# Kernel optimization log

Hardware: AMD Instinct MI355X
Metric: run time of the kernel (lower is better)

The kernel has to match this reference:

```python
import jax, jax.numpy as jnp
import numpy as np

TAU = 20.0   # membrane time constant (init default)
TH = 1.0     # spike threshold (init default)
K = 10.0     # surrogate sigmoid slope (hard-coded in forward)
EPS = 1e-6


def setup_inputs() -> dict:
    key = jax.random.key(0)
    I = jax.random.normal(key, (4096, 4096), dtype=jnp.float32)  # [B, L]
    return {"I": I}


def reference(I):
    B, L = I.shape

    def step(v, I_t):
        # Euler: dv = -v/tau + I ; v <- v + dv
        v = v - v / TAU + I_t
        s_soft = jax.nn.sigmoid(K * (v - TH))
        s_hard = (v >= TH).astype(I.dtype)
        # straight-through: value = s_hard, gradient flows through s_soft
        s = jax.lax.stop_gradient(s_hard - s_soft) + s_soft
        # reset: v <- v * (1 - stopgrad(s)); stopgrad(s) has value s_hard
        v = v * (1.0 - s_hard)
        return v, (s, s_hard)

    v0 = jnp.zeros((B,), dtype=I.dtype)
    _, (spikes_t, hard_t) = jax.lax.scan(step, v0, I.T)  # xs: [L, B]
    spikes = spikes_t.T       # [B, L]
    hard_spikes = hard_t.T    # [B, L]

    # hard latency: index of first hard spike, else L
    fired = hard_spikes > 0.5
    has = jnp.any(fired, axis=1)
    idx = jnp.argmax(fired, axis=1)
    hard_latency = jnp.where(has, idx, L).astype(jnp.int32)  # [B]

    # soft latency: spike-weighted mean time
    time = jnp.arange(L, dtype=spikes.dtype)
    w = spikes / (spikes.sum(axis=1, keepdims=True) + EPS)
    soft_latency = (w * time).sum(axis=1)  # [B]

    return spikes, hard_latency, soft_latency
```

## Files before the change

### kernel.cpp

```cpp
#include <hip/hip_runtime.h>

#define B_DIM 4096
#define L_DIM 4096
#define SEGLEN 256
#define NSEG (L_DIM / SEGLEN)
#define WARM 512
#define CHUNK 64
#define CF4 (CHUNK / 4)
#define LSTRIDE 68

__global__ __launch_bounds__(256) void init_kernel(float* wsf, int* wsi) {
    int i = blockIdx.x * 256 + threadIdx.x;
    if (i < 2 * B_DIM) wsf[i] = 0.f;
    if (i < B_DIM) wsi[i] = L_DIM;
}

#define LIF_CORE(IIN)                         \
    float q0 = u * cdiv;                      \
    float rr = fmaf(-20.0f, q0, u);           \
    float q  = fmaf(rr, cdiv, q0);            \
    float a  = u - q;                         \
    float b  = a + (IIN);                     \
    u = sp ? (IIN) : b;                       \
    sp = (u >= 1.0f);

#define WARM_STEP(IIN) { LIF_CORE(IIN) }

#define FULL_STEP(IIN, SOUT)                  \
    {                                         \
        LIF_CORE(IIN)                         \
        float sf = sp ? 1.0f : 0.0f;          \
        cnt += sf;                            \
        seen = fmaxf(seen, sf);               \
        accS += cnt;                          \
        accF += seen;                         \
        (SOUT) = sf;                          \
    }

__global__ __launch_bounds__(128, 1) void lif_kernel(const float* __restrict__ I,
                                                     float* __restrict__ out,
                                                     float* __restrict__ Cacc,
                                                     float* __restrict__ tsAcc,
                                                     int* __restrict__ firstAcc) {
    __shared__ __align__(16) float lds[2][64 * LSTRIDE];
    const int wid = threadIdx.x >> 6;
    const int lane = threadIdx.x & 63;
    const int seg = blockIdx.x >> 6;
    const int rowBase = (blockIdx.x & 63) * 64;
    const int t0 = seg * SEGLEN;
    const int start = (t0 > WARM) ? (t0 - WARM) : 0;
    const int nwarmCh = (t0 - start) / CHUNK;
    const int nch = nwarmCh + SEGLEN / CHUNK;

    if (wid == 1) {
        const int srow = lane >> 4, scol = lane & 15;
        const float* gb = I + (size_t)rowBase * L_DIM + start + scol * 4;
        {
            float* dst = &lds[0][0];
#pragma unroll
            for (int p = 0; p < 16; ++p) {
                const int r = 4 * p + srow;
                float4 v = *(const float4*)(gb + (size_t)r * L_DIM);
                *(float4*)&dst[r * LSTRIDE + scol * 4] = v;
            }
        }
        __syncthreads();
        for (int c = 0; c < nch; ++c) {
            if (c + 1 < nch) {
                const float* g = gb + (c + 1) * CHUNK;
                float* dst = &lds[(c + 1) & 1][0];
#pragma unroll
                for (int p = 0; p < 16; ++p) {
                    const int r = 4 * p + srow;
                    float4 v = *(const float4*)(g + (size_t)r * L_DIM);
                    *(float4*)&dst[r * LSTRIDE + scol * 4] = v;
                }
            }
            __syncthreads();
        }
    } else {
        const int row = rowBase + lane;
        float u = 0.f, cnt = 0.f, seen = 0.f, accS = 0.f, accF = 0.f;
        bool sp = false;
        const float cdiv = 0.05f;
        float* so = out + (size_t)row * L_DIM + t0;

        __syncthreads();
        for (int c = 0; c < nch; ++c) {
            const float* buf = &lds[c & 1][lane * LSTRIDE];
            float4 R[CF4];
#pragma unroll
            for (int j = 0; j < CF4; ++j) R[j] = *(const float4*)(buf + 4 * j);

            if (c < nwarmCh) {
#pragma unroll
                for (int j = 0; j < CF4; ++j) {
                    float4 iv = R[j];
                    WARM_STEP(iv.x) WARM_STEP(iv.y) WARM_STEP(iv.z) WARM_STEP(iv.w)
                }
            } else {
                float* sd = so + (c - nwarmCh) * CHUNK;
#pragma unroll
                for (int j = 0; j < CF4; ++j) {
                    float4 iv = R[j];
                    float4 sv;
                    FULL_STEP(iv.x, sv.x) FULL_STEP(iv.y, sv.y)
                    FULL_STEP(iv.z, sv.z) FULL_STEP(iv.w, sv.w)
                    *(float4*)(sd + 4 * j) = sv;
                }
            }
            __syncthreads();
        }

        if (cnt > 0.f) {
            const int firstLocal = (int)((float)SEGLEN - accF);
            atomicMin(&firstAcc[row], t0 + firstLocal);
        }
        atomicAdd(&Cacc[row], cnt);
        atomicAdd(&tsAcc[row], fmaf((float)(t0 + SEGLEN), cnt, -accS));
    }
}

__global__ __launch_bounds__(256) void fin_kernel(const float* __restrict__ Cacc,
                                                  const float* __restrict__ tsAcc,
                                                  const int* __restrict__ firstAcc,
                                                  float* __restrict__ out) {
    int r = blockIdx.x * 256 + threadIdx.x;
    if (r < B_DIM) {
        out[(size_t)B_DIM * L_DIM + r] = (float)firstAcc[r];
        out[(size_t)B_DIM * L_DIM + B_DIM + r] = tsAcc[r] / (Cacc[r] + 1e-6f);
    }
}

extern "C" void kernel_launch(void* const* d_in, const int* in_sizes, int n_in,
                              void* d_out, int out_size, void* d_ws, size_t ws_size,
                              hipStream_t stream) {
    const float* I = (const float*)d_in[0];
    float* out = (float*)d_out;
    float* wsf = (float*)d_ws;
    int* wsi = (int*)((float*)d_ws + 2 * B_DIM);
    (void)in_sizes; (void)n_in; (void)out_size; (void)ws_size;

    init_kernel<<<(2 * B_DIM + 255) / 256, 256, 0, stream>>>(wsf, wsi);
    lif_kernel<<<NSEG * 64, 128, 0, stream>>>(I, out, wsf, wsf + B_DIM, wsi);
    fin_kernel<<<(B_DIM + 255) / 256, 256, 0, stream>>>(wsf, wsf + B_DIM, wsi, out);
}
```

Before: 140.1 us.

## Stage spike outputs through LDS and store coalesced from the loader wave

Compute lanes now write spike values back into their LDS input buffer instead of storing straight to global memory with a per-row stride. On the next iteration the loader wave reads the finished chunk from LDS and writes it out as row-coalesced float4 stores, with a final flush after the loop. This is meant to replace strided, uncoalesced per-thread global stores with coalesced ones and take the store work off the compute wave. In exchange the loader wave does extra LDS traffic and more work between barriers, which may lengthen each synchronized step.

```diff
diff --git a/kernel.cpp b/kernel.cpp
--- a/kernel.cpp
+++ b/kernel.cpp
@@ -55,6 +55,7 @@
     if (wid == 1) {
         const int srow = lane >> 4, scol = lane & 15;
         const float* gb = I + (size_t)rowBase * L_DIM + start + scol * 4;
+        float* ob = out + (size_t)rowBase * L_DIM + t0 + scol * 4;
         {
             float* dst = &lds[0][0];
 #pragma unroll
@@ -66,6 +67,22 @@
         }
         __syncthreads();
         for (int c = 0; c < nch; ++c) {
+            const int cp = c - 1;
+            if (cp >= nwarmCh) {
+                float* sb = &lds[cp & 1][0];
+                float4 S[16];
+#pragma unroll
+                for (int p = 0; p < 16; ++p) {
+                    const int r = 4 * p + srow;
+                    S[p] = *(const float4*)&sb[r * LSTRIDE + scol * 4];
+                }
+                float* og = ob + (size_t)(cp - nwarmCh) * CHUNK;
+#pragma unroll
+                for (int p = 0; p < 16; ++p) {
+                    const int r = 4 * p + srow;
+                    *(float4*)(og + (size_t)r * L_DIM) = S[p];
+                }
+            }
             if (c + 1 < nch) {
                 const float* g = gb + (c + 1) * CHUNK;
                 float* dst = &lds[(c + 1) & 1][0];
@@ -78,16 +95,26 @@
             }
             __syncthreads();
         }
+        {
+            const int cp = nch - 1;
+            float* sb = &lds[cp & 1][0];
+            float* og = ob + (size_t)(cp - nwarmCh) * CHUNK;
+#pragma unroll
+            for (int p = 0; p < 16; ++p) {
+                const int r = 4 * p + srow;
+                float4 v = *(const float4*)&sb[r * LSTRIDE + scol * 4];
+                *(float4*)(og + (size_t)r * L_DIM) = v;
+            }
+        }
     } else {
         const int row = rowBase + lane;
         float u = 0.f, cnt = 0.f, seen = 0.f, accS = 0.f, accF = 0.f;
         bool sp = false;
         const float cdiv = 0.05f;
-        float* so = out + (size_t)row * L_DIM + t0;
 
         __syncthreads();
         for (int c = 0; c < nch; ++c) {
-            const float* buf = &lds[c & 1][lane * LSTRIDE];
+            float* buf = &lds[c & 1][lane * LSTRIDE];
             float4 R[CF4];
 #pragma unroll
             for (int j = 0; j < CF4; ++j) R[j] = *(const float4*)(buf + 4 * j);
@@ -99,14 +126,13 @@
                     WARM_STEP(iv.x) WARM_STEP(iv.y) WARM_STEP(iv.z) WARM_STEP(iv.w)
                 }
             } else {
-                float* sd = so + (c - nwarmCh) * CHUNK;
 #pragma unroll
                 for (int j = 0; j < CF4; ++j) {
                     float4 iv = R[j];
                     float4 sv;
                     FULL_STEP(iv.x, sv.x) FULL_STEP(iv.y, sv.y)
                     FULL_STEP(iv.z, sv.z) FULL_STEP(iv.w, sv.w)
-                    *(float4*)(sd + 4 * j) = sv;
+                    *(float4*)(buf + 4 * j) = sv;
                 }
             }
             __syncthreads();
```

New measurement: 129.9 us. 1.08x faster.

## Make each wave load, compute and store its own segment with register prefetch

Applied to the files above, without the earlier changes.

The producer/consumer wave split is replaced: each of the two waves in a block now handles its own time segment of the same 64 rows. Each wave prefetches the next chunk into registers, transposes through a private LDS buffer without block barriers, and writes spikes back through LDS as coalesced row-wise float4 stores. The goal is to double the number of compute waves, remove __syncthreads stalls and fix the strided per-lane output stores. In exchange it uses more registers per wave, and the extra LDS round-trips sit on the serial path.

```diff
diff --git a/kernel.cpp b/kernel.cpp
--- a/kernel.cpp
+++ b/kernel.cpp
@@ -45,80 +45,86 @@
     __shared__ __align__(16) float lds[2][64 * LSTRIDE];
     const int wid = threadIdx.x >> 6;
     const int lane = threadIdx.x & 63;
-    const int seg = blockIdx.x >> 6;
-    const int rowBase = (blockIdx.x & 63) * 64;
+    float* buf = &lds[wid][0];
+
+    const int rowBase = (blockIdx.x >> 3) * 64;
+    const int seg = ((blockIdx.x & 7) << 1) + wid;
     const int t0 = seg * SEGLEN;
     const int start = (t0 > WARM) ? (t0 - WARM) : 0;
     const int nwarmCh = (t0 - start) / CHUNK;
     const int nch = nwarmCh + SEGLEN / CHUNK;
 
-    if (wid == 1) {
-        const int srow = lane >> 4, scol = lane & 15;
-        const float* gb = I + (size_t)rowBase * L_DIM + start + scol * 4;
-        {
-            float* dst = &lds[0][0];
+    const int srow = lane >> 4, scol = lane & 15;
+    const float* gb = I + (size_t)rowBase * L_DIM + start + scol * 4;
+    float* ob = out + (size_t)rowBase * L_DIM + t0 + scol * 4;
+
+    const int row = rowBase + lane;
+    float u = 0.f, cnt = 0.f, seen = 0.f, accS = 0.f, accF = 0.f;
+    bool sp = false;
+    const float cdiv = 0.05f;
+
+    float4 G[16], R[16];
+
 #pragma unroll
-            for (int p = 0; p < 16; ++p) {
-                const int r = 4 * p + srow;
-                float4 v = *(const float4*)(gb + (size_t)r * L_DIM);
-                *(float4*)&dst[r * LSTRIDE + scol * 4] = v;
+    for (int p = 0; p < 16; ++p)
+        G[p] = *(const float4*)(gb + (size_t)(4 * p + srow) * L_DIM);
+#pragma unroll
+    for (int p = 0; p < 16; ++p)
+        *(float4*)&buf[(4 * p + srow) * LSTRIDE + scol * 4] = G[p];
+#pragma unroll
+    for (int j = 0; j < 16; ++j)
+        R[j] = *(const float4*)&buf[lane * LSTRIDE + 4 * j];
+
+    for (int c = 0; c < nch; ++c) {
+        if (c + 1 < nch) {
+            const float* g = gb + (c + 1) * CHUNK;
+#pragma unroll
+            for (int p = 0; p < 16; ++p)
+                G[p] = *(const float4*)(g + (size_t)(4 * p + srow) * L_DIM);
+        }
+        __builtin_amdgcn_sched_barrier(0);
+
+        if (c < nwarmCh) {
+#pragma unroll
+            for (int j = 0; j < 16; ++j) {
+                float4 iv = R[j];
+                WARM_STEP(iv.x) WARM_STEP(iv.y) WARM_STEP(iv.z) WARM_STEP(iv.w)
             }
-        }
-        __syncthreads();
-        for (int c = 0; c < nch; ++c) {
-            if (c + 1 < nch) {
-                const float* g = gb + (c + 1) * CHUNK;
-                float* dst = &lds[(c + 1) & 1][0];
+        } else {
 #pragma unroll
-                for (int p = 0; p < 16; ++p) {
-                    const int r = 4 * p + srow;
-                    float4 v = *(const float4*)(g + (size_t)r * L_DIM);
-                    *(float4*)&dst[r * LSTRIDE + scol * 4] = v;
-                }
+            for (int j = 0; j < 16; ++j) {
+                float4 iv = R[j];
+                float4 sv;
+                FULL_STEP(iv.x, sv.x) FULL_STEP(iv.y, sv.y)
+                FULL_STEP(iv.z, sv.z) FULL_STEP(iv.w, sv.w)
+                *(float4*)&buf[lane * LSTRIDE + 4 * j] = sv;
             }
-            __syncthreads();
-        }
-    } else {
-        const int row = rowBase + lane;
-        float u = 0.f, cnt = 0.f, seen = 0.f, accS = 0.f, accF = 0.f;
-        bool sp = false;
-        const float cdiv = 0.05f;
-        float* so = out + (size_t)row * L_DIM + t0;
-
-        __syncthreads();
-        for (int c = 0; c < nch; ++c) {
-            const float* buf = &lds[c & 1][lane * LSTRIDE];
-            float4 R[CF4];
+            float4 S[16];
+            float* og = ob + (size_t)(c - nwarmCh) * CHUNK;
 #pragma unroll
-            for (int j = 0; j < CF4; ++j) R[j] = *(const float4*)(buf + 4 * j);
-
-            if (c < nwarmCh) {
+            for (int p = 0; p < 16; ++p)
+                S[p] = *(const float4*)&buf[(4 * p + srow) * LSTRIDE + scol * 4];
 #pragma unroll
-                for (int j = 0; j < CF4; ++j) {
-                    float4 iv = R[j];
-                    WARM_STEP(iv.x) WARM_STEP(iv.y) WARM_STEP(iv.z) WARM_STEP(iv.w)
-                }
-            } else {
-                float* sd = so + (c - nwarmCh) * CHUNK;
-#pragma unroll
-                for (int j = 0; j < CF4; ++j) {
-                    float4 iv = R[j];
-                    float4 sv;
-                    FULL_STEP(iv.x, sv.x) FULL_STEP(iv.y, sv.y)
-                    FULL_STEP(iv.z, sv.z) FULL_STEP(iv.w, sv.w)
-                    *(float4*)(sd + 4 * j) = sv;
-                }
-            }
-            __syncthreads();
+            for (int p = 0; p < 16; ++p)
+                *(float4*)(og + (size_t)(4 * p + srow) * L_DIM) = S[p];
         }
 
-        if (cnt > 0.f) {
-            const int firstLocal = (int)((float)SEGLEN - accF);
-            atomicMin(&firstAcc[row], t0 + firstLocal);
+        if (c + 1 < nch) {
+#pragma unroll
+            for (int p = 0; p < 16; ++p)
+                *(float4*)&buf[(4 * p + srow) * LSTRIDE + scol * 4] = G[p];
+#pragma unroll
+            for (int j = 0; j < 16; ++j)
+                R[j] = *(const float4*)&buf[lane * LSTRIDE + 4 * j];
         }
-        atomicAdd(&Cacc[row], cnt);
-        atomicAdd(&tsAcc[row], fmaf((float)(t0 + SEGLEN), cnt, -accS));
     }
+
+    if (cnt > 0.f) {
+        const int firstLocal = (int)((float)SEGLEN - accF);
+        atomicMin(&firstAcc[row], t0 + firstLocal);
+    }
+    atomicAdd(&Cacc[row], cnt);
+    atomicAdd(&tsAcc[row], fmaf((float)(t0 + SEGLEN), cnt, -accS));
 }
 
 __global__ __launch_bounds__(256) void fin_kernel(const float* __restrict__ Cacc,
@@ -142,6 +148,6 @@
     (void)in_sizes; (void)n_in; (void)out_size; (void)ws_size;
 
     init_kernel<<<(2 * B_DIM + 255) / 256, 256, 0, stream>>>(wsf, wsi);
-    lif_kernel<<<NSEG * 64, 128, 0, stream>>>(I, out, wsf, wsf + B_DIM, wsi);
+    lif_kernel<<<(NSEG / 2) * 64, 128, 0, stream>>>(I, out, wsf, wsf + B_DIM, wsi);
     fin_kernel<<<(B_DIM + 255) / 256, 256, 0, stream>>>(wsf, wsf + B_DIM, wsi, out);
 }
```

Result: slower. 191.1 us (+36.4%).

## Use direct global-to-LDS loads so every wave computes its own segment

Applied to the files above, without the earlier changes.

The dedicated producer wave is removed. Each of the two waves in a block now handles its own time segment, prefetching the next chunk straight into LDS with global_load_lds in an XOR-swizzled layout and waiting on vmcnt instead of __syncthreads. Spike outputs are staged back through the LDS buffer so rows are written with coalesced float4 stores. Half as many blocks are launched, and the compute lanes per block double. The price is hand-tuned waitcnt logic that is fragile, plus wave-private LDS reuse that relies on in-order completion.

```diff
diff --git a/kernel.cpp b/kernel.cpp
--- a/kernel.cpp
+++ b/kernel.cpp
@@ -6,8 +6,7 @@
 #define NSEG (L_DIM / SEGLEN)
 #define WARM 512
 #define CHUNK 64
-#define CF4 (CHUNK / 4)
-#define LSTRIDE 68
+#define LROW 64
 
 __global__ __launch_bounds__(256) void init_kernel(float* wsf, int* wsi) {
     int i = blockIdx.x * 256 + threadIdx.x;
@@ -37,88 +36,116 @@
         (SOUT) = sf;                          \
     }
 
+typedef const __attribute__((address_space(1))) void g_void;
+typedef __attribute__((address_space(3))) void l_void;
+__device__ __forceinline__ void gll16(const float* src, float* ldsbase) {
+    __builtin_amdgcn_global_load_lds((g_void*)src, (l_void*)ldsbase, 16, 0, 0);
+}
+
 __global__ __launch_bounds__(128, 1) void lif_kernel(const float* __restrict__ I,
                                                      float* __restrict__ out,
                                                      float* __restrict__ Cacc,
                                                      float* __restrict__ tsAcc,
                                                      int* __restrict__ firstAcc) {
-    __shared__ __align__(16) float lds[2][64 * LSTRIDE];
+    __shared__ __align__(16) float lds[2][2][64 * LROW];
     const int wid = threadIdx.x >> 6;
     const int lane = threadIdx.x & 63;
-    const int seg = blockIdx.x >> 6;
-    const int rowBase = (blockIdx.x & 63) * 64;
+    float* buf0 = &lds[wid][0][0];
+    float* buf1 = &lds[wid][1][0];
+
+    const int rowBase = (blockIdx.x >> 3) * 64;
+    const int seg = ((blockIdx.x & 7) << 1) + wid;
     const int t0 = seg * SEGLEN;
     const int start = (t0 > WARM) ? (t0 - WARM) : 0;
     const int nwarmCh = (t0 - start) / CHUNK;
     const int nch = nwarmCh + SEGLEN / CHUNK;
 
-    if (wid == 1) {
-        const int srow = lane >> 4, scol = lane & 15;
-        const float* gb = I + (size_t)rowBase * L_DIM + start + scol * 4;
-        {
-            float* dst = &lds[0][0];
+    const int srow = lane >> 4, scol = lane & 15;
+    const float* gbase = I + (size_t)rowBase * L_DIM + start;
+
+    const int row = rowBase + lane;
+    float u = 0.f, cnt = 0.f, seen = 0.f, accS = 0.f, accF = 0.f;
+    bool sp = false;
+    const float cdiv = 0.05f;
+    float4 R[16];
+
+#define GLL_CHUNK(CC, DST)                                                  \
+    {                                                                       \
+        const float* gsrc = gbase + (size_t)(CC) * CHUNK;                   \
+        _Pragma("unroll")                                                   \
+        for (int p = 0; p < 16; ++p) {                                      \
+            const int r = 4 * p + srow;                                     \
+            gll16(gsrc + (size_t)r * L_DIM + (((scol - r) & 15) << 2),      \
+                  (DST) + p * 256);                                         \
+        }                                                                   \
+    }
+
+#define READ_R(SRC)                                                         \
+    {                                                                       \
+        _Pragma("unroll")                                                   \
+        for (int j = 0; j < 16; ++j)                                        \
+            R[j] = *(const float4*)&(SRC)[lane * LROW + (((j + lane) & 15) << 2)]; \
+    }
+
+    GLL_CHUNK(0, buf0)
+    asm volatile("s_waitcnt vmcnt(0)" ::: "memory");
+    __builtin_amdgcn_sched_barrier(0);
+    READ_R(buf0)
+
+    for (int c = 0; c < nch; ++c) {
+        float* bufc = (c & 1) ? buf1 : buf0;
+        float* bufn = (c & 1) ? buf0 : buf1;
+
+        if (c + 1 < nch) GLL_CHUNK(c + 1, bufn)
+        __builtin_amdgcn_sched_barrier(0);
+
+        if (c < nwarmCh) {
+#pragma unroll
+            for (int j = 0; j < 16; ++j) {
+                float4 iv = R[j];
+                WARM_STEP(iv.x) WARM_STEP(iv.y) WARM_STEP(iv.z) WARM_STEP(iv.w)
+            }
+        } else {
+#pragma unroll
+            for (int j = 0; j < 16; ++j) {
+                float4 iv = R[j];
+                float4 sv;
+                FULL_STEP(iv.x, sv.x) FULL_STEP(iv.y, sv.y)
+                FULL_STEP(iv.z, sv.z) FULL_STEP(iv.w, sv.w)
+                *(float4*)&bufc[lane * LROW + (((j + lane) & 15) << 2)] = sv;
+            }
+            float4 S[16];
+#pragma unroll
+            for (int p = 0; p < 16; ++p)
+                S[p] = *(const float4*)&bufc[p * 256 + lane * 4];
+            float* og = out + (size_t)rowBase * L_DIM + t0 +
+                        (size_t)(c - nwarmCh) * CHUNK;
 #pragma unroll
             for (int p = 0; p < 16; ++p) {
                 const int r = 4 * p + srow;
-                float4 v = *(const float4*)(gb + (size_t)r * L_DIM);
-                *(float4*)&dst[r * LSTRIDE + scol * 4] = v;
+                *(float4*)(og + (size_t)r * L_DIM + (((scol - r) & 15) << 2)) = S[p];
             }
         }
-        __syncthreads();
-        for (int c = 0; c < nch; ++c) {
-            if (c + 1 < nch) {
-                const float* g = gb + (c + 1) * CHUNK;
-                float* dst = &lds[(c + 1) & 1][0];
-#pragma unroll
-                for (int p = 0; p < 16; ++p) {
-                    const int r = 4 * p + srow;
-                    float4 v = *(const float4*)(g + (size_t)r * L_DIM);
-                    *(float4*)&dst[r * LSTRIDE + scol * 4] = v;
-                }
+
+        if (c + 1 < nch) {
+            if (c >= nwarmCh) {
+                asm volatile("s_waitcnt vmcnt(16)" ::: "memory");
+            } else {
+                asm volatile("s_waitcnt vmcnt(0)" ::: "memory");
             }
-            __syncthreads();
+            __builtin_amdgcn_sched_barrier(0);
+            READ_R(bufn)
         }
-    } else {
-        const int row = rowBase + lane;
-        float u = 0.f, cnt = 0.f, seen = 0.f, accS = 0.f, accF = 0.f;
-        bool sp = false;
-        const float cdiv = 0.05f;
-        float* so = out + (size_t)row * L_DIM + t0;
+    }
 
-        __syncthreads();
-        for (int c = 0; c < nch; ++c) {
-            const float* buf = &lds[c & 1][lane * LSTRIDE];
-            float4 R[CF4];
-#pragma unroll
-            for (int j = 0; j < CF4; ++j) R[j] = *(const float4*)(buf + 4 * j);
-
-            if (c < nwarmCh) {
-#pragma unroll
-                for (int j = 0; j < CF4; ++j) {
-                    float4 iv = R[j];
-                    WARM_STEP(iv.x) WARM_STEP(iv.y) WARM_STEP(iv.z) WARM_STEP(iv.w)
-                }
-            } else {
-                float* sd = so + (c - nwarmCh) * CHUNK;
-#pragma unroll
-                for (int j = 0; j < CF4; ++j) {
-                    float4 iv = R[j];
-                    float4 sv;
-                    FULL_STEP(iv.x, sv.x) FULL_STEP(iv.y, sv.y)
-                    FULL_STEP(iv.z, sv.z) FULL_STEP(iv.w, sv.w)
-                    *(float4*)(sd + 4 * j) = sv;
-                }
-            }
-            __syncthreads();
-        }
-
-        if (cnt > 0.f) {
-            const int firstLocal = (int)((float)SEGLEN - accF);
-            atomicMin(&firstAcc[row], t0 + firstLocal);
-        }
-        atomicAdd(&Cacc[row], cnt);
-        atomicAdd(&tsAcc[row], fmaf((float)(t0 + SEGLEN), cnt, -accS));
+    if (cnt > 0.f) {
+        const int firstLocal = (int)((float)SEGLEN - accF);
+        atomicMin(&firstAcc[row], t0 + firstLocal);
     }
+    atomicAdd(&Cacc[row], cnt);
+    atomicAdd(&tsAcc[row], fmaf((float)(t0 + SEGLEN), cnt, -accS));
+#undef GLL_CHUNK
+#undef READ_R
 }
 
 __global__ __launch_bounds__(256) void fin_kernel(const float* __restrict__ Cacc,
@@ -142,6 +169,6 @@
     (void)in_sizes; (void)n_in; (void)out_size; (void)ws_size;
 
     init_kernel<<<(2 * B_DIM + 255) / 256, 256, 0, stream>>>(wsf, wsi);
-    lif_kernel<<<NSEG * 64, 128, 0, stream>>>(I, out, wsf, wsf + B_DIM, wsi);
+    lif_kernel<<<(B_DIM / 64) * (NSEG / 2), 128, 0, stream>>>(I, out, wsf, wsf + B_DIM, wsi);
     fin_kernel<<<(B_DIM + 255) / 256, 256, 0, stream>>>(wsf, wsf + B_DIM, wsi, out);
 }
```

Result: no change. 137.9 us (-1.5%).
